# Performance work log

Measured on AMD Instinct MI355X. Metric: run time of the kernel, lower is better.

The kernel has to match this reference:

```python
import jax, jax.numpy as jnp
import numpy as np

LAMBDA_RECON = 1.0
LAMBDA_IF = 0.5
LAMBDA_SMOOTH = 0.1

B, N, T = 8, 8, 262144


def setup_inputs() -> dict:
    key = jax.random.key(0)
    ks = jax.random.split(key, 7)
    return {
        "recon_real": jax.random.normal(ks[0], (B, T), dtype=jnp.float32),
        "recon_imag": jax.random.normal(ks[1], (B, T), dtype=jnp.float32),
        "target_real": jax.random.normal(ks[2], (B, T), dtype=jnp.float32),
        "target_imag": jax.random.normal(ks[3], (B, T), dtype=jnp.float32),
        "eIF": jax.random.normal(ks[4], (B, N, T), dtype=jnp.float32),
        "target_if": jax.random.normal(ks[5], (B, N, T), dtype=jnp.float32),
        "mode_mask": jax.random.randint(ks[6], (B, N), 0, 2, dtype=jnp.int32),
    }


def _mse(a, b):
    d = a - b
    return jnp.mean(d * d)


def reference(recon_real, recon_imag, target_real, target_imag, eIF, target_if, mode_mask):
    # reconstruction loss: MSE on real part + MSE on imag part
    recon_loss = _mse(recon_real, target_real) + _mse(recon_imag, target_imag)
    total_loss = LAMBDA_RECON * recon_loss

    # IF loss: mask broadcast over time axis, MSE of masked tensors
    maskf = (mode_mask == 1).astype(eIF.dtype)          # [B, N]
    valid = maskf[:, :, None]                            # [B, N, 1] broadcasts over T
    if_loss = _mse(eIF * valid, target_if * valid)
    total_loss = total_loss + LAMBDA_IF * if_loss

    # smoothness: mean of per-(b,n) mean squared temporal diff, over masked modes
    if_diff = eIF[:, :, 1:] - eIF[:, :, :-1]             # [B, N, T-1]
    per_mode = jnp.mean(if_diff * if_diff, axis=-1)      # [B, N]
    count = jnp.sum(maskf)
    smooth_loss = jnp.sum(per_mode * maskf) / jnp.maximum(count, 1.0)
    # original skips smooth term if no mode is active
    smooth_term = jnp.where(count > 0, LAMBDA_SMOOTH * smooth_loss, 0.0)
    total_loss = total_loss + smooth_term

    return total_loss, recon_loss, if_loss, smooth_loss
```

## Files before the change

kernel.cpp:

```cpp
#include <hip/hip_runtime.h>


namespace {
constexpr int    kB = 8;
constexpr int    kN = 8;
constexpr int    kT = 262144;
constexpr long long kBT  = (long long)kB * kT;
constexpr long long kBNT = (long long)kB * kN * kT;

constexpr int THREADS     = 256;
constexpr int GRID        = 2048;
constexpr int RECON_UNITS = 2048;
constexpr int IF_SEGS     = 64;
constexpr int IF_UNITS    = kB * kN * IF_SEGS;

constexpr double LAMBDA_IF     = 0.5;
constexpr double LAMBDA_SMOOTH = 0.1;
}

__device__ __forceinline__ float sq(float x) { return x * x; }

__device__ __forceinline__ void recon_accum(int u, int tid,
                                            const float4* __restrict__ rr4,
                                            const float4* __restrict__ tr4,
                                            const float4* __restrict__ ri4,
                                            const float4* __restrict__ ti4,
                                            float& a0, float& a1) {
    const int v = u * THREADS + tid;
    float4 x = rr4[v], y = tr4[v];
    float4 m = ri4[v], w = ti4[v];
    a0 += sq(x.x - y.x) + sq(x.y - y.y) + sq(x.z - y.z) + sq(x.w - y.w);
    a1 += sq(m.x - w.x) + sq(m.y - w.y) + sq(m.z - w.z) + sq(m.w - w.w);
}

__device__ __forceinline__ void if_accum(int iu, int tid,
                                         const float* __restrict__ eIF,
                                         const float* __restrict__ tIF,
                                         const int* __restrict__ smask,
                                         float& a2, float& a3) {
    const int row = iu >> 6;
    const int seg = iu & (IF_SEGS - 1);
    if (smask[row] != 1) return;

    const float4* e4 = (const float4*)(eIF + (size_t)row * kT);
    const float4* t4 = (const float4*)(tIF + (size_t)row * kT);
    constexpr int VPR = kT / 4;
    const int base = seg * 1024 + tid;
    const int b0 = base, b1 = base + 256, b2 = base + 512, b3 = base + 768;
    const bool lane63 = (tid & 63) == 63;

    float4 e0 = e4[b0], e1 = e4[b1], e2 = e4[b2], e3 = e4[b3];
    float4 q0 = t4[b0], q1 = t4[b1], q2 = t4[b2], q3 = t4[b3];
    float n0 = 0.f, n1 = 0.f, n2 = 0.f, n3 = 0.f;
    if (lane63) {
        n0 = e4[b0 + 1].x;
        n1 = e4[b1 + 1].x;
        n2 = e4[b2 + 1].x;
        n3 = (b3 + 1 < VPR) ? e4[b3 + 1].x : e3.w;
    }
    a2 += sq(e0.x - q0.x) + sq(e0.y - q0.y) + sq(e0.z - q0.z) + sq(e0.w - q0.w)
        + sq(e1.x - q1.x) + sq(e1.y - q1.y) + sq(e1.z - q1.z) + sq(e1.w - q1.w)
        + sq(e2.x - q2.x) + sq(e2.y - q2.y) + sq(e2.z - q2.z) + sq(e2.w - q2.w)
        + sq(e3.x - q3.x) + sq(e3.y - q3.y) + sq(e3.z - q3.z) + sq(e3.w - q3.w);
    a3 += sq(e0.y - e0.x) + sq(e0.z - e0.y) + sq(e0.w - e0.z)
        + sq(e1.y - e1.x) + sq(e1.z - e1.y) + sq(e1.w - e1.z)
        + sq(e2.y - e2.x) + sq(e2.z - e2.y) + sq(e2.w - e2.z)
        + sq(e3.y - e3.x) + sq(e3.z - e3.y) + sq(e3.w - e3.z);
    float s0 = __shfl_down(e0.x, 1, 64);
    float s1 = __shfl_down(e1.x, 1, 64);
    float s2 = __shfl_down(e2.x, 1, 64);
    float s3 = __shfl_down(e3.x, 1, 64);
    if (lane63) { s0 = n0; s1 = n1; s2 = n2; s3 = n3; }
    a3 += sq(s0 - e0.w) + sq(s1 - e1.w) + sq(s2 - e2.w) + sq(s3 - e3.w);
}

__global__ __launch_bounds__(THREADS, 8)
void vncmd_main_kernel(const float* __restrict__ rr, const float* __restrict__ ri,
                       const float* __restrict__ tr, const float* __restrict__ ti,
                       const float* __restrict__ eIF, const float* __restrict__ tIF,
                       const int* __restrict__ mask, double* __restrict__ ws) {
    const int tid = threadIdx.x;
    const int bid = blockIdx.x;

    __shared__ int smask[kB * kN];
    if (tid < kB * kN) smask[tid] = mask[tid];
    __syncthreads();

    float a0 = 0.f, a1 = 0.f, a2 = 0.f, a3 = 0.f;
    recon_accum(bid, tid, (const float4*)rr, (const float4*)tr,
                (const float4*)ri, (const float4*)ti, a0, a1);
    if_accum(bid,        tid, eIF, tIF, smask, a2, a3);
    if_accum(bid + 2048, tid, eIF, tIF, smask, a2, a3);

    double d0 = (double)a0, d1 = (double)a1, d2 = (double)a2, d3 = (double)a3;
    #pragma unroll
    for (int o = 32; o > 0; o >>= 1) {
        d0 += __shfl_down(d0, o, 64);
        d1 += __shfl_down(d1, o, 64);
        d2 += __shfl_down(d2, o, 64);
        d3 += __shfl_down(d3, o, 64);
    }
    __shared__ double lds[4][4];
    const int lane = tid & 63;
    const int wid  = tid >> 6;
    if (lane == 0) { lds[wid][0] = d0; lds[wid][1] = d1; lds[wid][2] = d2; lds[wid][3] = d3; }
    __syncthreads();
    if (tid == 0) {
        double* dst = ws + 4 * bid;
        dst[0] = lds[0][0] + lds[1][0] + lds[2][0] + lds[3][0];
        dst[1] = lds[0][1] + lds[1][1] + lds[2][1] + lds[3][1];
        dst[2] = lds[0][2] + lds[1][2] + lds[2][2] + lds[3][2];
        dst[3] = lds[0][3] + lds[1][3] + lds[2][3] + lds[3][3];
    }
}

__global__ __launch_bounds__(THREADS)
void finalize_kernel(const double* __restrict__ ws,
                     const int* __restrict__ mask,
                     float* __restrict__ out) {
    const int tid = threadIdx.x;
    const double2* w2 = (const double2*)ws;
    double s0 = 0.0, s1 = 0.0, s2 = 0.0, s3 = 0.0;
    #pragma unroll
    for (int k = 0; k < GRID / THREADS; ++k) {
        const int b = k * THREADS + tid;
        double2 p = w2[2 * b], q = w2[2 * b + 1];
        s0 += p.x; s1 += p.y; s2 += q.x; s3 += q.y;
    }
    #pragma unroll
    for (int o = 32; o > 0; o >>= 1) {
        s0 += __shfl_down(s0, o, 64);
        s1 += __shfl_down(s1, o, 64);
        s2 += __shfl_down(s2, o, 64);
        s3 += __shfl_down(s3, o, 64);
    }
    __shared__ double lds[4][4];
    const int lane = tid & 63;
    const int wid  = tid >> 6;
    if (lane == 0) { lds[wid][0] = s0; lds[wid][1] = s1; lds[wid][2] = s2; lds[wid][3] = s3; }
    __syncthreads();
    if (tid == 0) {
        double t0 = lds[0][0] + lds[1][0] + lds[2][0] + lds[3][0];
        double t1 = lds[0][1] + lds[1][1] + lds[2][1] + lds[3][1];
        double t2 = lds[0][2] + lds[1][2] + lds[2][2] + lds[3][2];
        double t3 = lds[0][3] + lds[1][3] + lds[2][3] + lds[3][3];
        int c = 0;
        #pragma unroll
        for (int i = 0; i < kB * kN; ++i) c += (mask[i] == 1);
        double count = (double)c;
        double recon = t0 / (double)kBT + t1 / (double)kBT;
        double ifl   = t2 / (double)kBNT;
        double denom = (count > 1.0 ? count : 1.0) * (double)(kT - 1);
        double smooth = t3 / denom;
        double total = recon + LAMBDA_IF * ifl + (count > 0.0 ? LAMBDA_SMOOTH * smooth : 0.0);
        out[0] = (float)total;
        out[1] = (float)recon;
        out[2] = (float)ifl;
        out[3] = (float)smooth;
    }
}

extern "C" void kernel_launch(void* const* d_in, const int* in_sizes, int n_in,
                              void* d_out, int out_size, void* d_ws, size_t ws_size,
                              hipStream_t stream) {
    const float* rr  = (const float*)d_in[0];
    const float* ri  = (const float*)d_in[1];
    const float* tr  = (const float*)d_in[2];
    const float* ti  = (const float*)d_in[3];
    const float* eIF = (const float*)d_in[4];
    const float* tIF = (const float*)d_in[5];
    const int*   msk = (const int*)d_in[6];
    float* out = (float*)d_out;
    double* ws = (double*)d_ws;

    vncmd_main_kernel<<<GRID, THREADS, 0, stream>>>(
        rr, ri, tr, ti, eIF, tIF, msk, ws);
    finalize_kernel<<<1, THREADS, 0, stream>>>(ws, msk, out);
}
```

Baseline: 24.82 us.

## Compact active IF rows and distribute work units evenly across blocks

Builds a compacted list of active mask rows with a wavefront ballot, then assigns recon units and active IF segments to blocks through a grid-stride loop. The intent is to remove the load imbalance where blocks mapped to masked-out rows idle while others do two IF segments. Recon units now cover twice as many elements each. The finalize kernel uses 1024 threads, so each thread does fewer serial partial-sum reads. The loop adds a branch and a dynamic trip count per block.

```diff
diff --git a/kernel.cpp b/kernel.cpp
--- a/kernel.cpp
+++ b/kernel.cpp
@@ -10,9 +10,8 @@
 
 constexpr int THREADS     = 256;
 constexpr int GRID        = 2048;
-constexpr int RECON_UNITS = 2048;
+constexpr int RECON_UNITS = 1024;
 constexpr int IF_SEGS     = 64;
-constexpr int IF_UNITS    = kB * kN * IF_SEGS;
 
 constexpr double LAMBDA_IF     = 0.5;
 constexpr double LAMBDA_SMOOTH = 0.1;
@@ -20,77 +19,78 @@
 
 __device__ __forceinline__ float sq(float x) { return x * x; }
 
-__device__ __forceinline__ void recon_accum(int u, int tid,
-                                            const float4* __restrict__ rr4,
-                                            const float4* __restrict__ tr4,
-                                            const float4* __restrict__ ri4,
-                                            const float4* __restrict__ ti4,
-                                            float& a0, float& a1) {
-    const int v = u * THREADS + tid;
-    float4 x = rr4[v], y = tr4[v];
-    float4 m = ri4[v], w = ti4[v];
-    a0 += sq(x.x - y.x) + sq(x.y - y.y) + sq(x.z - y.z) + sq(x.w - y.w);
-    a1 += sq(m.x - w.x) + sq(m.y - w.y) + sq(m.z - w.z) + sq(m.w - w.w);
-}
-
-__device__ __forceinline__ void if_accum(int iu, int tid,
-                                         const float* __restrict__ eIF,
-                                         const float* __restrict__ tIF,
-                                         const int* __restrict__ smask,
-                                         float& a2, float& a3) {
-    const int row = iu >> 6;
-    const int seg = iu & (IF_SEGS - 1);
-    if (smask[row] != 1) return;
-
-    const float4* e4 = (const float4*)(eIF + (size_t)row * kT);
-    const float4* t4 = (const float4*)(tIF + (size_t)row * kT);
-    constexpr int VPR = kT / 4;
-    const int base = seg * 1024 + tid;
-    const int b0 = base, b1 = base + 256, b2 = base + 512, b3 = base + 768;
-    const bool lane63 = (tid & 63) == 63;
-
-    float4 e0 = e4[b0], e1 = e4[b1], e2 = e4[b2], e3 = e4[b3];
-    float4 q0 = t4[b0], q1 = t4[b1], q2 = t4[b2], q3 = t4[b3];
-    float n0 = 0.f, n1 = 0.f, n2 = 0.f, n3 = 0.f;
-    if (lane63) {
-        n0 = e4[b0 + 1].x;
-        n1 = e4[b1 + 1].x;
-        n2 = e4[b2 + 1].x;
-        n3 = (b3 + 1 < VPR) ? e4[b3 + 1].x : e3.w;
-    }
-    a2 += sq(e0.x - q0.x) + sq(e0.y - q0.y) + sq(e0.z - q0.z) + sq(e0.w - q0.w)
-        + sq(e1.x - q1.x) + sq(e1.y - q1.y) + sq(e1.z - q1.z) + sq(e1.w - q1.w)
-        + sq(e2.x - q2.x) + sq(e2.y - q2.y) + sq(e2.z - q2.z) + sq(e2.w - q2.w)
-        + sq(e3.x - q3.x) + sq(e3.y - q3.y) + sq(e3.z - q3.z) + sq(e3.w - q3.w);
-    a3 += sq(e0.y - e0.x) + sq(e0.z - e0.y) + sq(e0.w - e0.z)
-        + sq(e1.y - e1.x) + sq(e1.z - e1.y) + sq(e1.w - e1.z)
-        + sq(e2.y - e2.x) + sq(e2.z - e2.y) + sq(e2.w - e2.z)
-        + sq(e3.y - e3.x) + sq(e3.z - e3.y) + sq(e3.w - e3.z);
-    float s0 = __shfl_down(e0.x, 1, 64);
-    float s1 = __shfl_down(e1.x, 1, 64);
-    float s2 = __shfl_down(e2.x, 1, 64);
-    float s3 = __shfl_down(e3.x, 1, 64);
-    if (lane63) { s0 = n0; s1 = n1; s2 = n2; s3 = n3; }
-    a3 += sq(s0 - e0.w) + sq(s1 - e1.w) + sq(s2 - e2.w) + sq(s3 - e3.w);
-}
-
 __global__ __launch_bounds__(THREADS, 8)
 void vncmd_main_kernel(const float* __restrict__ rr, const float* __restrict__ ri,
                        const float* __restrict__ tr, const float* __restrict__ ti,
                        const float* __restrict__ eIF, const float* __restrict__ tIF,
                        const int* __restrict__ mask, double* __restrict__ ws) {
-    const int tid = threadIdx.x;
-    const int bid = blockIdx.x;
+    const int tid  = threadIdx.x;
+    const int bid  = blockIdx.x;
+    const int lane = tid & 63;
+    const int wid  = tid >> 6;
 
-    __shared__ int smask[kB * kN];
-    if (tid < kB * kN) smask[tid] = mask[tid];
+    __shared__ int s_active[kB * kN];
+    __shared__ int s_U;
+    if (tid < 64) {
+        const int m = mask[tid];
+        const unsigned long long bits = __ballot(m == 1);
+        const int pos = (int)__popcll(bits & ((1ull << lane) - 1ull));
+        if (m == 1) s_active[pos] = lane;
+        if (lane == 0) s_U = RECON_UNITS + IF_SEGS * (int)__popcll(bits);
+    }
     __syncthreads();
+    const int U = s_U;
 
     float a0 = 0.f, a1 = 0.f, a2 = 0.f, a3 = 0.f;
-    recon_accum(bid, tid, (const float4*)rr, (const float4*)tr,
-                (const float4*)ri, (const float4*)ti, a0, a1);
-    if_accum(bid,        tid, eIF, tIF, smask, a2, a3);
-    if_accum(bid + 2048, tid, eIF, tIF, smask, a2, a3);
+    for (int u = bid; u < U; u += GRID) {
+        if (u < RECON_UNITS) {
+            const float4* rr4 = (const float4*)rr;
+            const float4* tr4 = (const float4*)tr;
+            const float4* ri4 = (const float4*)ri;
+            const float4* ti4 = (const float4*)ti;
+            const int v0 = u * 512 + tid, v1 = v0 + 256;
+            float4 x0 = rr4[v0], x1 = rr4[v1], y0 = tr4[v0], y1 = tr4[v1];
+            float4 m0 = ri4[v0], m1 = ri4[v1], w0 = ti4[v0], w1 = ti4[v1];
+            a0 += sq(x0.x - y0.x) + sq(x0.y - y0.y) + sq(x0.z - y0.z) + sq(x0.w - y0.w)
+                + sq(x1.x - y1.x) + sq(x1.y - y1.y) + sq(x1.z - y1.z) + sq(x1.w - y1.w);
+            a1 += sq(m0.x - w0.x) + sq(m0.y - w0.y) + sq(m0.z - w0.z) + sq(m0.w - w0.w)
+                + sq(m1.x - w1.x) + sq(m1.y - w1.y) + sq(m1.z - w1.z) + sq(m1.w - w1.w);
+        } else {
+            const int au  = u - RECON_UNITS;
+            const int row = s_active[au >> 6];
+            const int seg = au & (IF_SEGS - 1);
+            const float4* e4 = (const float4*)(eIF + (size_t)row * kT);
+            const float4* t4 = (const float4*)(tIF + (size_t)row * kT);
+            constexpr int VPR = kT / 4;
+            const int base = seg * 1024 + tid;
+            const int b0 = base, b1 = base + 256, b2 = base + 512, b3 = base + 768;
+            const bool l63 = (lane == 63);
+
+            float4 e0 = e4[b0], e1 = e4[b1], e2 = e4[b2], e3 = e4[b3];
+            float4 q0 = t4[b0], q1 = t4[b1], q2 = t4[b2], q3 = t4[b3];
+            float n0 = 0.f, n1 = 0.f, n2 = 0.f, n3 = 0.f;
+            if (l63) {
+                n0 = e4[b0 + 1].x;
+                n1 = e4[b1 + 1].x;
+                n2 = e4[b2 + 1].x;
+                n3 = (b3 + 1 < VPR) ? e4[b3 + 1].x : e3.w;
+            }
+            a2 += sq(e0.x - q0.x) + sq(e0.y - q0.y) + sq(e0.z - q0.z) + sq(e0.w - q0.w)
+                + sq(e1.x - q1.x) + sq(e1.y - q1.y) + sq(e1.z - q1.z) + sq(e1.w - q1.w)
+                + sq(e2.x - q2.x) + sq(e2.y - q2.y) + sq(e2.z - q2.z) + sq(e2.w - q2.w)
+                + sq(e3.x - q3.x) + sq(e3.y - q3.y) + sq(e3.z - q3.z) + sq(e3.w - q3.w);
+            a3 += sq(e0.y - e0.x) + sq(e0.z - e0.y) + sq(e0.w - e0.z)
+                + sq(e1.y - e1.x) + sq(e1.z - e1.y) + sq(e1.w - e1.z)
+                + sq(e2.y - e2.x) + sq(e2.z - e2.y) + sq(e2.w - e2.z)
+                + sq(e3.y - e3.x) + sq(e3.z - e3.y) + sq(e3.w - e3.z);
+            float s0 = __shfl_down(e0.x, 1, 64);
+            float s1 = __shfl_down(e1.x, 1, 64);
+            float s2 = __shfl_down(e2.x, 1, 64);
+            float s3 = __shfl_down(e3.x, 1, 64);
+            if (l63) { s0 = n0; s1 = n1; s2 = n2; s3 = n3; }
+            a3 += sq(s0 - e0.w) + sq(s1 - e1.w) + sq(s2 - e2.w) + sq(s3 - e3.w);
+        }
+    }
 
     double d0 = (double)a0, d1 = (double)a1, d2 = (double)a2, d3 = (double)a3;
     #pragma unroll
@@ -101,8 +101,6 @@
         d3 += __shfl_down(d3, o, 64);
     }
     __shared__ double lds[4][4];
-    const int lane = tid & 63;
-    const int wid  = tid >> 6;
     if (lane == 0) { lds[wid][0] = d0; lds[wid][1] = d1; lds[wid][2] = d2; lds[wid][3] = d3; }
     __syncthreads();
     if (tid == 0) {
@@ -114,16 +112,19 @@
     }
 }
 
-__global__ __launch_bounds__(THREADS)
+__global__ __launch_bounds__(1024)
 void finalize_kernel(const double* __restrict__ ws,
                      const int* __restrict__ mask,
                      float* __restrict__ out) {
-    const int tid = threadIdx.x;
+    const int tid  = threadIdx.x;
+    const int lane = tid & 63;
+    const int wid  = tid >> 6;
+
     const double2* w2 = (const double2*)ws;
     double s0 = 0.0, s1 = 0.0, s2 = 0.0, s3 = 0.0;
     #pragma unroll
-    for (int k = 0; k < GRID / THREADS; ++k) {
-        const int b = k * THREADS + tid;
+    for (int k = 0; k < GRID / 1024; ++k) {
+        const int b = k * 1024 + tid;
         double2 p = w2[2 * b], q = w2[2 * b + 1];
         s0 += p.x; s1 += p.y; s2 += q.x; s3 += q.y;
     }
@@ -134,16 +135,15 @@
         s2 += __shfl_down(s2, o, 64);
         s3 += __shfl_down(s3, o, 64);
     }
-    __shared__ double lds[4][4];
-    const int lane = tid & 63;
-    const int wid  = tid >> 6;
+    __shared__ double lds[16][4];
     if (lane == 0) { lds[wid][0] = s0; lds[wid][1] = s1; lds[wid][2] = s2; lds[wid][3] = s3; }
     __syncthreads();
     if (tid == 0) {
-        double t0 = lds[0][0] + lds[1][0] + lds[2][0] + lds[3][0];
-        double t1 = lds[0][1] + lds[1][1] + lds[2][1] + lds[3][1];
-        double t2 = lds[0][2] + lds[1][2] + lds[2][2] + lds[3][2];
-        double t3 = lds[0][3] + lds[1][3] + lds[2][3] + lds[3][3];
+        double t0 = 0.0, t1 = 0.0, t2 = 0.0, t3 = 0.0;
+        #pragma unroll
+        for (int i = 0; i < 16; ++i) {
+            t0 += lds[i][0]; t1 += lds[i][1]; t2 += lds[i][2]; t3 += lds[i][3];
+        }
         int c = 0;
         #pragma unroll
         for (int i = 0; i < kB * kN; ++i) c += (mask[i] == 1);
@@ -175,5 +175,5 @@
 
     vncmd_main_kernel<<<GRID, THREADS, 0, stream>>>(
         rr, ri, tr, ti, eIF, tIF, msk, ws);
-    finalize_kernel<<<1, THREADS, 0, stream>>>(ws, msk, out);
+    finalize_kernel<<<1, 1024, 0, stream>>>(ws, msk, out);
 }
```

New measurement: 26.35 us. +6.2%, slower.
